# Optimization experiments

Measured on AMD Instinct MI355X. Metric: run time of the kernel, lower is better.

Reference implementation:

```python
import jax, jax.numpy as jnp
import numpy as np

NUM_ITEMS = 100000
EMB_DIM = 128
HALF = EMB_DIM // 2
MAX_ITEMS = 200
BATCH = 16384


def setup_inputs() -> dict:
    key = jax.random.key(0)
    ks = jax.random.split(key, 16)
    inp = {
        "ratings": jax.random.uniform(ks[0], (BATCH, MAX_ITEMS), jnp.float32) * 5.0,
        "item_ids": jax.random.randint(ks[1], (BATCH, MAX_ITEMS), 0, NUM_ITEMS),
        "noise": jax.random.normal(ks[2], (BATCH, EMB_DIM), jnp.float32),
        "init_user_emb": jax.random.normal(ks[3], (BATCH, EMB_DIM), jnp.float32),
        # embedding tables (embedding_dim=4)
        "gmf_emb": jax.random.normal(ks[4], (NUM_ITEMS, 4), jnp.float32) * 0.1,
        "ncf_emb": jax.random.normal(ks[5], (NUM_ITEMS, 4), jnp.float32) * 0.1,
        # four Linear(HALF, 4) layers (kaiming-normal-ish weights, zero bias)
        "W0": jax.random.normal(ks[6], (4, HALF), jnp.float32) * np.sqrt(2.0 / 4),
        "b0": jnp.zeros((4,), jnp.float32),
        "W1": jax.random.normal(ks[7], (4, HALF), jnp.float32) * np.sqrt(2.0 / 4),
        "b1": jnp.zeros((4,), jnp.float32),
        "W2": jax.random.normal(ks[8], (4, HALF), jnp.float32) * np.sqrt(2.0 / 4),
        "b2": jnp.zeros((4,), jnp.float32),
        "W3": jax.random.normal(ks[9], (4, HALF), jnp.float32) * np.sqrt(2.0 / 4),
        "b3": jnp.zeros((4,), jnp.float32),
        # ncf_layers: Linear(12, 8) + ReLU
        "Wn": jax.random.normal(ks[10], (8, 12), jnp.float32) * 0.2,
        "bn": jnp.zeros((8,), jnp.float32),
        # final_layer: Linear(16, 1)
        "Wf": jax.random.normal(ks[11], (1, 16), jnp.float32) * 0.2,
        "bf": jnp.zeros((1,), jnp.float32),
        # learned mixing scalar p
        "p": jnp.ones((1,), jnp.float32),
    }
    return inp


def _forward(ratings, item_ids, noise, init_user_emb,
             gmf_emb, ncf_emb, W0, b0, W1, b1, W2, b2, W3, b3,
             Wn, bn, Wf, bf, p):
    # embedding lookups: [B, M, 4]
    gmf_item = gmf_emb[item_ids]
    ncf_item = ncf_emb[item_ids]
    # split user emb / noise into gmf, ncf halves: [B, HALF] each
    gmf_user, ncf_user = init_user_emb[:, :HALF], init_user_emb[:, HALF:]
    gmf_noise, ncf_noise = noise[:, :HALF], noise[:, HALF:]
    # tiny projections to dim 4
    gmf_user = gmf_user @ W0.T + b0        # [B, 4]
    ncf_user = ncf_user @ W1.T + b1        # [B, 4]
    gmf_noise = gmf_noise @ W2.T + b2      # [B, 4]
    ncf_noise = ncf_noise @ W3.T + b3      # [B, 4]
    # einsum 'ijk,ik->ijk': elementwise scale by broadcast
    gmf_noise_e = gmf_item * gmf_noise[:, None, :]   # [B, M, 4]
    gmf_user_e = gmf_item * gmf_user[:, None, :]     # [B, M, 4]
    gmf_out = jnp.concatenate([gmf_user_e, gmf_noise_e], axis=-1)  # [B, M, 8]
    # broadcast ncf user/noise over items, concat with item embs: [B, M, 12]
    B, M = item_ids.shape
    ncf_in = jnp.concatenate([
        jnp.broadcast_to(ncf_user[:, None, :], (B, M, 4)),
        jnp.broadcast_to(ncf_noise[:, None, :], (B, M, 4)),
        ncf_item,
    ], axis=-1)
    ncf_out = jax.nn.relu(ncf_in @ Wn.T + bn)        # [B, M, 8]
    comb = jnp.concatenate([gmf_out, ncf_out], axis=-1)  # [B, M, 16]
    score = (comb @ Wf.T + bf)[..., 0]               # [B, M]
    return p * ratings + score


def reference(ratings, item_ids, noise, init_user_emb,
              gmf_emb, ncf_emb, W0, b0, W1, b1, W2, b2, W3, b3,
              Wn, bn, Wf, bf, p):
    return _forward(ratings, item_ids, noise, init_user_emb,
                    gmf_emb, ncf_emb, W0, b0, W1, b1, W2, b2, W3, b3,
                    Wn, bn, Wf, bf, p)
```

## Files before the change

kernel.cpp:

```cpp
#include <hip/hip_runtime.h>
#include <hip/hip_bf16.h>

#define BATCH 16384
#define MAX_ITEMS 200
#define TOTAL (BATCH * MAX_ITEMS)
#define NUM_ITEMS 100000
#define A_USERS 64
#define PREP_A_BLOCKS (BATCH / A_USERS)
#define PACK_BLOCKS ((NUM_ITEMS + 255) / 256)

typedef _Float16 half8 __attribute__((ext_vector_type(8)));
typedef float    f32x4 __attribute__((ext_vector_type(4)));
typedef int      i32x4 __attribute__((ext_vector_type(4)));

__global__ __launch_bounds__(256) void prep(
    const float* __restrict__ noise,
    const float* __restrict__ uemb,
    const float* __restrict__ gmf_emb,
    const float* __restrict__ ncf_emb,
    const float* __restrict__ W0, const float* __restrict__ b0,
    const float* __restrict__ W1, const float* __restrict__ b1,
    const float* __restrict__ W2, const float* __restrict__ b2,
    const float* __restrict__ W3, const float* __restrict__ b3,
    const float* __restrict__ Wn, const float* __restrict__ bn,
    const float* __restrict__ Wf,
    float* __restrict__ consts,
    half8* __restrict__ packed)
{
    const int tid = threadIdx.x;

    if (blockIdx.x >= PREP_A_BLOCKS) {
        int i = (blockIdx.x - PREP_A_BLOCKS) * 256 + tid;
        if (i < NUM_ITEMS) {
            float4 g = reinterpret_cast<const float4*>(gmf_emb)[i];
            float4 c = reinterpret_cast<const float4*>(ncf_emb)[i];
            half8 z;
            z[0] = (_Float16)g.x; z[1] = (_Float16)g.y;
            z[2] = (_Float16)g.z; z[3] = (_Float16)g.w;
            z[4] = (_Float16)c.x; z[5] = (_Float16)c.y;
            z[6] = (_Float16)c.z; z[7] = (_Float16)c.w;
            packed[i] = z;
        }
        return;
    }

    __shared__ float sIn[A_USERS * 260];
    __shared__ float sW[16 * 68];
    __shared__ float sproj[A_USERS * 17];

    const int ub = blockIdx.x * A_USERS;

    for (int k = tid; k < 1024; k += 256) {
        int row = k >> 6, i = k & 63;
        int r = row >> 2, j = row & 3;
        const float* Wr = (r == 0) ? W0 : (r == 1) ? W1 : (r == 2) ? W2 : W3;
        sW[row * 68 + i] = Wr[j * 64 + i];
    }

    const float4* ue4 = reinterpret_cast<const float4*>(uemb  + (size_t)ub * 128);
    const float4* no4 = reinterpret_cast<const float4*>(noise + (size_t)ub * 128);
#pragma unroll
    for (int it = 0; it < 8; ++it) {
        int k   = it * 256 + tid;
        int u_l = k >> 5, seg = k & 31;
        float4 v = ue4[k];
        float4 w = no4[k];
        *reinterpret_cast<float4*>(&sIn[u_l * 260 + seg * 4])       = v;
        *reinterpret_cast<float4*>(&sIn[u_l * 260 + 128 + seg * 4]) = w;
    }
    __syncthreads();

    const int u_local = tid >> 2;
    const int r       = tid & 3;
    const float4* src = reinterpret_cast<const float4*>(&sIn[u_local * 260 + r * 64]);
    const float4* w0p = reinterpret_cast<const float4*>(&sW[(r * 4 + 0) * 68]);
    const float4* w1p = reinterpret_cast<const float4*>(&sW[(r * 4 + 1) * 68]);
    const float4* w2p = reinterpret_cast<const float4*>(&sW[(r * 4 + 2) * 68]);
    const float4* w3p = reinterpret_cast<const float4*>(&sW[(r * 4 + 3) * 68]);

    float a0 = 0.f, a1 = 0.f, a2 = 0.f, a3 = 0.f;
#pragma unroll
    for (int i4 = 0; i4 < 16; ++i4) {
        float4 x  = src[i4];
        float4 w0 = w0p[i4];
        float4 w1 = w1p[i4];
        float4 w2 = w2p[i4];
        float4 w3 = w3p[i4];
        a0 += x.x * w0.x + x.y * w0.y + x.z * w0.z + x.w * w0.w;
        a1 += x.x * w1.x + x.y * w1.y + x.z * w1.z + x.w * w1.w;
        a2 += x.x * w2.x + x.y * w2.y + x.z * w2.z + x.w * w2.w;
        a3 += x.x * w3.x + x.y * w3.y + x.z * w3.z + x.w * w3.w;
    }
    const float* br = (r == 0) ? b0 : (r == 1) ? b1 : (r == 2) ? b2 : b3;
    sproj[u_local * 17 + r * 4 + 0] = a0 + br[0];
    sproj[u_local * 17 + r * 4 + 1] = a1 + br[1];
    sproj[u_local * 17 + r * 4 + 2] = a2 + br[2];
    sproj[u_local * 17 + r * 4 + 3] = a3 + br[3];
    __syncthreads();

    if (tid < A_USERS) {
        float pr[16];
#pragma unroll
        for (int c = 0; c < 16; ++c) pr[c] = sproj[tid * 17 + c];

        float uu[4], base[8];
#pragma unroll
        for (int j = 0; j < 4; ++j)
            uu[j] = Wf[j] * pr[j] + Wf[4 + j] * pr[8 + j];
#pragma unroll
        for (int k = 0; k < 8; ++k) {
            float t = bn[k];
#pragma unroll
            for (int i = 0; i < 4; ++i)
                t += Wn[k * 12 + i] * pr[4 + i] + Wn[k * 12 + 4 + i] * pr[12 + i];
            base[k] = t;
        }
        float4* o = reinterpret_cast<float4*>(consts + (size_t)(ub + tid) * 12);
        o[0] = make_float4(uu[0], uu[1], uu[2], uu[3]);
        o[1] = make_float4(base[0], base[1], base[2], base[3]);
        o[2] = make_float4(base[4], base[5], base[6], base[7]);
    }
}

__global__ __launch_bounds__(256) void score4(
    const float* __restrict__ ratings,
    const int*   __restrict__ ids,
    const half8* __restrict__ packed,
    const float* __restrict__ Wn,
    const float* __restrict__ Wf,
    const float* __restrict__ bf,
    const float* __restrict__ p,
    const float* __restrict__ consts,
    float* __restrict__ out)
{
    __shared__ float sWn[32];
    __shared__ float sWf[8];
    __shared__ float sBF, sP;

    const int tid = threadIdx.x;
    if (tid < 32)       sWn[tid] = Wn[(tid >> 2) * 12 + 8 + (tid & 3)];
    else if (tid < 40)  sWf[tid - 32] = Wf[8 + (tid - 32)];
    else if (tid == 40) sBF = bf[0];
    else if (tid == 41) sP  = p[0];
    __syncthreads();

    const int t = blockIdx.x * 256 + tid;
    const int u = t / (MAX_ITEMS / 4);

    f32x4 r4  = __builtin_nontemporal_load(reinterpret_cast<const f32x4*>(ratings) + t);
    i32x4 id4 = __builtin_nontemporal_load(reinterpret_cast<const i32x4*>(ids) + t);

    half8 z0 = packed[id4.x];
    half8 z1 = packed[id4.y];
    half8 z2 = packed[id4.z];
    half8 z3 = packed[id4.w];

    const float4* cu = reinterpret_cast<const float4*>(consts + (size_t)u * 12);
    float4 c0 = cu[0];
    float4 c1 = cu[1];
    float4 c2 = cu[2];
    const float base[8] = {c1.x, c1.y, c1.z, c1.w, c2.x, c2.y, c2.z, c2.w};

    const half8 zs[4] = {z0, z1, z2, z3};
    const float rr[4] = {r4.x, r4.y, r4.z, r4.w};
    float res[4];

#pragma unroll
    for (int e = 0; e < 4; ++e) {
        half8 z = zs[e];
        float gx = (float)z[0], gy = (float)z[1], gz = (float)z[2], gw = (float)z[3];
        float nx = (float)z[4], ny = (float)z[5], nz = (float)z[6], nw = (float)z[7];
        float acc = sBF + gx * c0.x + gy * c0.y + gz * c0.z + gw * c0.w;
#pragma unroll
        for (int k = 0; k < 8; ++k) {
            float tv = base[k]
                     + sWn[k * 4 + 0] * nx
                     + sWn[k * 4 + 1] * ny
                     + sWn[k * 4 + 2] * nz
                     + sWn[k * 4 + 3] * nw;
            acc += sWf[k] * fmaxf(tv, 0.0f);
        }
        res[e] = sP * rr[e] + acc;
    }

    f32x4 o4;
    o4.x = res[0]; o4.y = res[1]; o4.z = res[2]; o4.w = res[3];
    __builtin_nontemporal_store(o4, reinterpret_cast<f32x4*>(out) + t);
}

extern "C" void kernel_launch(void* const* d_in, const int* in_sizes, int n_in,
                              void* d_out, int out_size, void* d_ws, size_t ws_size,
                              hipStream_t stream) {
    const float* ratings = (const float*)d_in[0];
    const int*   ids     = (const int*)  d_in[1];
    const float* noise   = (const float*)d_in[2];
    const float* uemb    = (const float*)d_in[3];
    const float* gmf_emb = (const float*)d_in[4];
    const float* ncf_emb = (const float*)d_in[5];
    const float* W0 = (const float*)d_in[6];
    const float* b0 = (const float*)d_in[7];
    const float* W1 = (const float*)d_in[8];
    const float* b1 = (const float*)d_in[9];
    const float* W2 = (const float*)d_in[10];
    const float* b2 = (const float*)d_in[11];
    const float* W3 = (const float*)d_in[12];
    const float* b3 = (const float*)d_in[13];
    const float* Wn = (const float*)d_in[14];
    const float* bn = (const float*)d_in[15];
    const float* Wf = (const float*)d_in[16];
    const float* bf = (const float*)d_in[17];
    const float* p  = (const float*)d_in[18];
    float* out = (float*)d_out;

    half8* packed = (half8*)d_ws;
    float* consts = (float*)((char*)d_ws + (1u << 21));

    prep<<<PREP_A_BLOCKS + PACK_BLOCKS, 256, 0, stream>>>(
        noise, uemb, gmf_emb, ncf_emb,
        W0, b0, W1, b1, W2, b2, W3, b3, Wn, bn, Wf, consts, packed);

    score4<<<TOTAL / 4 / 256, 256, 0, stream>>>(
        ratings, ids, packed, Wn, Wf, bf, p, consts, out);
}
```

Before: 139.7 us.

## Fuse per-user projection into scoring kernel, split item packing into own kernel

Moves the per-user projection (user/noise through W0-W3, then through Wn/Wf) out of the prep kernel and into the scoring kernel. Each block now handles 4 users (200 threads active for items) and computes their constants in shared memory, so the consts buffer no longer makes a round trip through global memory. Item packing becomes its own small kernel, and the gathers of packed items now use nontemporal loads. In exchange there are extra __syncthreads, 56 of 256 threads sit idle, and each block repeats the weight loads.

```diff
diff --git a/kernel.cpp b/kernel.cpp
--- a/kernel.cpp
+++ b/kernel.cpp
@@ -5,187 +5,175 @@
 #define MAX_ITEMS 200
 #define TOTAL (BATCH * MAX_ITEMS)
 #define NUM_ITEMS 100000
-#define A_USERS 64
-#define PREP_A_BLOCKS (BATCH / A_USERS)
 #define PACK_BLOCKS ((NUM_ITEMS + 255) / 256)
 
 typedef _Float16 half8 __attribute__((ext_vector_type(8)));
 typedef float    f32x4 __attribute__((ext_vector_type(4)));
 typedef int      i32x4 __attribute__((ext_vector_type(4)));
 
-__global__ __launch_bounds__(256) void prep(
+__global__ __launch_bounds__(256) void pack_items(
+    const float* __restrict__ gmf_emb,
+    const float* __restrict__ ncf_emb,
+    half8* __restrict__ packed)
+{
+    int i = blockIdx.x * 256 + threadIdx.x;
+    if (i >= NUM_ITEMS) return;
+    float4 g = reinterpret_cast<const float4*>(gmf_emb)[i];
+    float4 c = reinterpret_cast<const float4*>(ncf_emb)[i];
+    half8 z;
+    z[0] = (_Float16)g.x; z[1] = (_Float16)g.y;
+    z[2] = (_Float16)g.z; z[3] = (_Float16)g.w;
+    z[4] = (_Float16)c.x; z[5] = (_Float16)c.y;
+    z[6] = (_Float16)c.z; z[7] = (_Float16)c.w;
+    packed[i] = z;
+}
+
+__global__ __launch_bounds__(256) void score_fused(
+    const float* __restrict__ ratings,
+    const int*   __restrict__ ids,
+    const half8* __restrict__ packed,
     const float* __restrict__ noise,
     const float* __restrict__ uemb,
-    const float* __restrict__ gmf_emb,
-    const float* __restrict__ ncf_emb,
     const float* __restrict__ W0, const float* __restrict__ b0,
     const float* __restrict__ W1, const float* __restrict__ b1,
     const float* __restrict__ W2, const float* __restrict__ b2,
     const float* __restrict__ W3, const float* __restrict__ b3,
     const float* __restrict__ Wn, const float* __restrict__ bn,
-    const float* __restrict__ Wf,
-    float* __restrict__ consts,
-    half8* __restrict__ packed)
-{
-    const int tid = threadIdx.x;
-
-    if (blockIdx.x >= PREP_A_BLOCKS) {
-        int i = (blockIdx.x - PREP_A_BLOCKS) * 256 + tid;
-        if (i < NUM_ITEMS) {
-            float4 g = reinterpret_cast<const float4*>(gmf_emb)[i];
-            float4 c = reinterpret_cast<const float4*>(ncf_emb)[i];
-            half8 z;
-            z[0] = (_Float16)g.x; z[1] = (_Float16)g.y;
-            z[2] = (_Float16)g.z; z[3] = (_Float16)g.w;
-            z[4] = (_Float16)c.x; z[5] = (_Float16)c.y;
-            z[6] = (_Float16)c.z; z[7] = (_Float16)c.w;
-            packed[i] = z;
-        }
-        return;
-    }
-
-    __shared__ float sIn[A_USERS * 260];
-    __shared__ float sW[16 * 68];
-    __shared__ float sproj[A_USERS * 17];
-
-    const int ub = blockIdx.x * A_USERS;
-
-    for (int k = tid; k < 1024; k += 256) {
-        int row = k >> 6, i = k & 63;
-        int r = row >> 2, j = row & 3;
-        const float* Wr = (r == 0) ? W0 : (r == 1) ? W1 : (r == 2) ? W2 : W3;
-        sW[row * 68 + i] = Wr[j * 64 + i];
-    }
-
-    const float4* ue4 = reinterpret_cast<const float4*>(uemb  + (size_t)ub * 128);
-    const float4* no4 = reinterpret_cast<const float4*>(noise + (size_t)ub * 128);
-#pragma unroll
-    for (int it = 0; it < 8; ++it) {
-        int k   = it * 256 + tid;
-        int u_l = k >> 5, seg = k & 31;
-        float4 v = ue4[k];
-        float4 w = no4[k];
-        *reinterpret_cast<float4*>(&sIn[u_l * 260 + seg * 4])       = v;
-        *reinterpret_cast<float4*>(&sIn[u_l * 260 + 128 + seg * 4]) = w;
-    }
-    __syncthreads();
-
-    const int u_local = tid >> 2;
-    const int r       = tid & 3;
-    const float4* src = reinterpret_cast<const float4*>(&sIn[u_local * 260 + r * 64]);
-    const float4* w0p = reinterpret_cast<const float4*>(&sW[(r * 4 + 0) * 68]);
-    const float4* w1p = reinterpret_cast<const float4*>(&sW[(r * 4 + 1) * 68]);
-    const float4* w2p = reinterpret_cast<const float4*>(&sW[(r * 4 + 2) * 68]);
-    const float4* w3p = reinterpret_cast<const float4*>(&sW[(r * 4 + 3) * 68]);
-
-    float a0 = 0.f, a1 = 0.f, a2 = 0.f, a3 = 0.f;
-#pragma unroll
-    for (int i4 = 0; i4 < 16; ++i4) {
-        float4 x  = src[i4];
-        float4 w0 = w0p[i4];
-        float4 w1 = w1p[i4];
-        float4 w2 = w2p[i4];
-        float4 w3 = w3p[i4];
-        a0 += x.x * w0.x + x.y * w0.y + x.z * w0.z + x.w * w0.w;
-        a1 += x.x * w1.x + x.y * w1.y + x.z * w1.z + x.w * w1.w;
-        a2 += x.x * w2.x + x.y * w2.y + x.z * w2.z + x.w * w2.w;
-        a3 += x.x * w3.x + x.y * w3.y + x.z * w3.z + x.w * w3.w;
-    }
-    const float* br = (r == 0) ? b0 : (r == 1) ? b1 : (r == 2) ? b2 : b3;
-    sproj[u_local * 17 + r * 4 + 0] = a0 + br[0];
-    sproj[u_local * 17 + r * 4 + 1] = a1 + br[1];
-    sproj[u_local * 17 + r * 4 + 2] = a2 + br[2];
-    sproj[u_local * 17 + r * 4 + 3] = a3 + br[3];
-    __syncthreads();
-
-    if (tid < A_USERS) {
-        float pr[16];
-#pragma unroll
-        for (int c = 0; c < 16; ++c) pr[c] = sproj[tid * 17 + c];
-
-        float uu[4], base[8];
-#pragma unroll
-        for (int j = 0; j < 4; ++j)
-            uu[j] = Wf[j] * pr[j] + Wf[4 + j] * pr[8 + j];
-#pragma unroll
-        for (int k = 0; k < 8; ++k) {
-            float t = bn[k];
-#pragma unroll
-            for (int i = 0; i < 4; ++i)
-                t += Wn[k * 12 + i] * pr[4 + i] + Wn[k * 12 + 4 + i] * pr[12 + i];
-            base[k] = t;
-        }
-        float4* o = reinterpret_cast<float4*>(consts + (size_t)(ub + tid) * 12);
-        o[0] = make_float4(uu[0], uu[1], uu[2], uu[3]);
-        o[1] = make_float4(base[0], base[1], base[2], base[3]);
-        o[2] = make_float4(base[4], base[5], base[6], base[7]);
-    }
-}
-
-__global__ __launch_bounds__(256) void score4(
-    const float* __restrict__ ratings,
-    const int*   __restrict__ ids,
-    const half8* __restrict__ packed,
-    const float* __restrict__ Wn,
-    const float* __restrict__ Wf,
-    const float* __restrict__ bf,
+    const float* __restrict__ Wf, const float* __restrict__ bf,
     const float* __restrict__ p,
-    const float* __restrict__ consts,
     float* __restrict__ out)
 {
+    __shared__ float sIn[4 * 264];
+    __shared__ float sPart[4 * 4 * 16];
+    __shared__ float sproj[4 * 17];
+    __shared__ float sConsts[4 * 12];
     __shared__ float sWn[32];
     __shared__ float sWf[8];
     __shared__ float sBF, sP;
 
     const int tid = threadIdx.x;
+    const int ub  = blockIdx.x * 4;
+
+    f32x4 r4 = {0.f, 0.f, 0.f, 0.f};
+    i32x4 id4 = {0, 0, 0, 0};
+    const int t = blockIdx.x * 200 + tid;
+    if (tid < 200) {
+        r4  = __builtin_nontemporal_load(reinterpret_cast<const f32x4*>(ratings) + t);
+        id4 = __builtin_nontemporal_load(reinterpret_cast<const i32x4*>(ids) + t);
+    }
+
+    if (tid < 128) {
+        int u_l = tid >> 5, seg = tid & 31;
+        float4 v = reinterpret_cast<const float4*>(uemb + (size_t)ub * 128)[tid];
+        *reinterpret_cast<float4*>(&sIn[u_l * 264 + seg * 4]) = v;
+    } else {
+        int k = tid - 128;
+        int u_l = k >> 5, seg = k & 31;
+        float4 v = reinterpret_cast<const float4*>(noise + (size_t)ub * 128)[k];
+        *reinterpret_cast<float4*>(&sIn[u_l * 264 + 128 + seg * 4]) = v;
+    }
     if (tid < 32)       sWn[tid] = Wn[(tid >> 2) * 12 + 8 + (tid & 3)];
     else if (tid < 40)  sWf[tid - 32] = Wf[8 + (tid - 32)];
     else if (tid == 40) sBF = bf[0];
     else if (tid == 41) sP  = p[0];
     __syncthreads();
 
-    const int t = blockIdx.x * 256 + tid;
-    const int u = t / (MAX_ITEMS / 4);
-
-    f32x4 r4  = __builtin_nontemporal_load(reinterpret_cast<const f32x4*>(ratings) + t);
-    i32x4 id4 = __builtin_nontemporal_load(reinterpret_cast<const i32x4*>(ids) + t);
-
-    half8 z0 = packed[id4.x];
-    half8 z1 = packed[id4.y];
-    half8 z2 = packed[id4.z];
-    half8 z3 = packed[id4.w];
-
-    const float4* cu = reinterpret_cast<const float4*>(consts + (size_t)u * 12);
-    float4 c0 = cu[0];
-    float4 c1 = cu[1];
-    float4 c2 = cu[2];
-    const float base[8] = {c1.x, c1.y, c1.z, c1.w, c2.x, c2.y, c2.z, c2.w};
-
-    const half8 zs[4] = {z0, z1, z2, z3};
-    const float rr[4] = {r4.x, r4.y, r4.z, r4.w};
-    float res[4];
-
-#pragma unroll
-    for (int e = 0; e < 4; ++e) {
-        half8 z = zs[e];
-        float gx = (float)z[0], gy = (float)z[1], gz = (float)z[2], gw = (float)z[3];
-        float nx = (float)z[4], ny = (float)z[5], nz = (float)z[6], nw = (float)z[7];
-        float acc = sBF + gx * c0.x + gy * c0.y + gz * c0.z + gw * c0.w;
+    if (tid < 64) {
+        int u_l = tid >> 4, r = (tid >> 2) & 3, q = tid & 3;
+        const float* Wr = (r == 0) ? W0 : (r == 1) ? W1 : (r == 2) ? W2 : W3;
+        const float4* x4 = reinterpret_cast<const float4*>(&sIn[u_l * 264 + r * 64 + q * 16]);
+        float s0 = 0.f, s1 = 0.f, s2 = 0.f, s3 = 0.f;
+#pragma unroll
+        for (int i4 = 0; i4 < 4; ++i4) {
+            float4 x  = x4[i4];
+            float4 w0 = reinterpret_cast<const float4*>(Wr + 0 * 64 + q * 16)[i4];
+            float4 w1 = reinterpret_cast<const float4*>(Wr + 1 * 64 + q * 16)[i4];
+            float4 w2 = reinterpret_cast<const float4*>(Wr + 2 * 64 + q * 16)[i4];
+            float4 w3 = reinterpret_cast<const float4*>(Wr + 3 * 64 + q * 16)[i4];
+            s0 += x.x * w0.x + x.y * w0.y + x.z * w0.z + x.w * w0.w;
+            s1 += x.x * w1.x + x.y * w1.y + x.z * w1.z + x.w * w1.w;
+            s2 += x.x * w2.x + x.y * w2.y + x.z * w2.z + x.w * w2.w;
+            s3 += x.x * w3.x + x.y * w3.y + x.z * w3.z + x.w * w3.w;
+        }
+        int b = (u_l * 4 + r) * 16;
+        sPart[b + 0 * 4 + q] = s0;
+        sPart[b + 1 * 4 + q] = s1;
+        sPart[b + 2 * 4 + q] = s2;
+        sPart[b + 3 * 4 + q] = s3;
+    }
+    __syncthreads();
+
+    if (tid < 64) {
+        int u_l = tid >> 4, r = (tid >> 2) & 3, j = tid & 3;
+        const float* br = (r == 0) ? b0 : (r == 1) ? b1 : (r == 2) ? b2 : b3;
+        int b = (u_l * 4 + r) * 16 + j * 4;
+        sproj[u_l * 17 + r * 4 + j] =
+            sPart[b + 0] + sPart[b + 1] + sPart[b + 2] + sPart[b + 3] + br[j];
+    }
+    __syncthreads();
+
+    if (tid < 4) {
+        float pr[16];
+#pragma unroll
+        for (int c = 0; c < 16; ++c) pr[c] = sproj[tid * 17 + c];
+        float* o = &sConsts[tid * 12];
+#pragma unroll
+        for (int j = 0; j < 4; ++j)
+            o[j] = Wf[j] * pr[j] + Wf[4 + j] * pr[8 + j];
 #pragma unroll
         for (int k = 0; k < 8; ++k) {
-            float tv = base[k]
-                     + sWn[k * 4 + 0] * nx
-                     + sWn[k * 4 + 1] * ny
-                     + sWn[k * 4 + 2] * nz
-                     + sWn[k * 4 + 3] * nw;
-            acc += sWf[k] * fmaxf(tv, 0.0f);
+            float s = bn[k];
+#pragma unroll
+            for (int i = 0; i < 4; ++i)
+                s += Wn[k * 12 + i] * pr[4 + i] + Wn[k * 12 + 4 + i] * pr[12 + i];
+            o[4 + k] = s;
         }
-        res[e] = sP * rr[e] + acc;
-    }
-
-    f32x4 o4;
-    o4.x = res[0]; o4.y = res[1]; o4.z = res[2]; o4.w = res[3];
-    __builtin_nontemporal_store(o4, reinterpret_cast<f32x4*>(out) + t);
+    }
+    __syncthreads();
+
+    if (tid < 200) {
+        const int u_l = tid / 50;
+        const float* cw = &sConsts[u_l * 12];
+        const float c0x = cw[0], c0y = cw[1], c0z = cw[2], c0w = cw[3];
+        float base[8];
+#pragma unroll
+        for (int k = 0; k < 8; ++k) base[k] = cw[4 + k];
+
+        const i32x4* ptab = reinterpret_cast<const i32x4*>(packed);
+        i32x4 zz0 = __builtin_nontemporal_load(ptab + id4.x);
+        i32x4 zz1 = __builtin_nontemporal_load(ptab + id4.y);
+        i32x4 zz2 = __builtin_nontemporal_load(ptab + id4.z);
+        i32x4 zz3 = __builtin_nontemporal_load(ptab + id4.w);
+        half8 z0 = __builtin_bit_cast(half8, zz0);
+        half8 z1 = __builtin_bit_cast(half8, zz1);
+        half8 z2 = __builtin_bit_cast(half8, zz2);
+        half8 z3 = __builtin_bit_cast(half8, zz3);
+
+        const half8 zs[4] = {z0, z1, z2, z3};
+        const float rr[4] = {r4.x, r4.y, r4.z, r4.w};
+        float res[4];
+#pragma unroll
+        for (int e = 0; e < 4; ++e) {
+            half8 z = zs[e];
+            float gx = (float)z[0], gy = (float)z[1], gz = (float)z[2], gw = (float)z[3];
+            float nx = (float)z[4], ny = (float)z[5], nz = (float)z[6], nw = (float)z[7];
+            float acc = sBF + gx * c0x + gy * c0y + gz * c0z + gw * c0w;
+#pragma unroll
+            for (int k = 0; k < 8; ++k) {
+                float tv = base[k]
+                         + sWn[k * 4 + 0] * nx
+                         + sWn[k * 4 + 1] * ny
+                         + sWn[k * 4 + 2] * nz
+                         + sWn[k * 4 + 3] * nw;
+                acc += sWf[k] * fmaxf(tv, 0.0f);
+            }
+            res[e] = sP * rr[e] + acc;
+        }
+
+        f32x4 o4;
+        o4.x = res[0]; o4.y = res[1]; o4.z = res[2]; o4.w = res[3];
+        __builtin_nontemporal_store(o4, reinterpret_cast<f32x4*>(out) + t);
+    }
 }
 
 extern "C" void kernel_launch(void* const* d_in, const int* in_sizes, int n_in,
@@ -213,12 +201,10 @@
     float* out = (float*)d_out;
 
     half8* packed = (half8*)d_ws;
-    float* consts = (float*)((char*)d_ws + (1u << 21));
-
-    prep<<<PREP_A_BLOCKS + PACK_BLOCKS, 256, 0, stream>>>(
-        noise, uemb, gmf_emb, ncf_emb,
-        W0, b0, W1, b1, W2, b2, W3, b3, Wn, bn, Wf, consts, packed);
-
-    score4<<<TOTAL / 4 / 256, 256, 0, stream>>>(
-        ratings, ids, packed, Wn, Wf, bf, p, consts, out);
+
+    pack_items<<<PACK_BLOCKS, 256, 0, stream>>>(gmf_emb, ncf_emb, packed);
+
+    score_fused<<<BATCH / 4, 256, 0, stream>>>(
+        ratings, ids, packed, noise, uemb,
+        W0, b0, W1, b1, W2, b2, W3, b3, Wn, bn, Wf, bf, p, out);
 }
```

Result: slower. 159.8 us (+14.4%).
